# Kernel tuning notes

Measured on AMD Instinct MI355X. Metric: run time of the kernel, lower is better.

## Reference

```python
import jax, jax.numpy as jnp
import numpy as np

B, T, D = 4, 1024, 1024
H = 16                      # attention heads
DS, DC, EXP = 16, 4, 2      # d_state, d_conv, expand
DIN = EXP * D               # 2048
DTR = D // 16               # dt_rank = 64
TOPK_RATIO = 0.25
EPS = 1e-5


def setup_inputs() -> dict:
    key = jax.random.key(0)
    ks = jax.random.split(key, 16)
    def n(k, shape, scale=0.02):
        return jax.random.normal(k, shape, jnp.float32) * scale
    return {
        "x": jax.random.normal(ks[0], (B, T, D), jnp.float32),
        "ln_w": jnp.ones((D,), jnp.float32),
        "ln_b": jnp.zeros((D,), jnp.float32),
        "r_w1": n(ks[1], (D, D // 2)),
        "r_b1": jnp.zeros((D // 2,), jnp.float32),
        "r_w2": n(ks[2], (D // 2, 1)),
        "r_b2": jnp.zeros((1,), jnp.float32),
        "Wq": n(ks[3], (D, D)), "bq": jnp.zeros((D,), jnp.float32),
        "Wk": n(ks[4], (D, D)), "bk": jnp.zeros((D,), jnp.float32),
        "Wv": n(ks[5], (D, D)), "bv": jnp.zeros((D,), jnp.float32),
        "Wo": n(ks[6], (D, D)), "bo": jnp.zeros((D,), jnp.float32),
        "in_w": n(ks[7], (D, 2 * DIN)),
        "conv_w": n(ks[8], (DIN, DC), 0.1),
        "conv_b": jnp.zeros((DIN,), jnp.float32),
        "xproj_w": n(ks[9], (DIN, DTR + 2 * DS)),
        "dt_w": n(ks[10], (DTR, DIN), 0.1),
        "dt_b": jnp.full((DIN,), -4.0, jnp.float32) + n(ks[11], (DIN,), 0.1),
        "A_log": jnp.log(jnp.broadcast_to(jnp.arange(1, DS + 1, dtype=jnp.float32), (DIN, DS))),
        "Dp": jnp.ones((DIN,), jnp.float32),
        "out_w": n(ks[12], (DIN, D)),
    }


def _attn_core(x, Wq, bq, Wk, bk, Wv, bv, Wo, bo):
    b, L, d = x.shape
    hd = d // H
    q = (x @ Wq + bq).reshape(b, L, H, hd)
    k = (x @ Wk + bk).reshape(b, L, H, hd)
    v = (x @ Wv + bv).reshape(b, L, H, hd)
    scores = jnp.einsum('bqhd,bkhd->bhqk', q, k) / jnp.sqrt(jnp.float32(hd))
    p = jax.nn.softmax(scores, axis=-1)
    o = jnp.einsum('bhqk,bkhd->bqhd', p, v).reshape(b, L, d)
    return o @ Wo + bo


def _ssm_core(u, in_w, conv_w, conv_b, xproj_w, dt_w, dt_b, A_log, Dp, out_w):
    # Mamba-style selective SSM on the sub-sequence u: (b, L, D)
    b, L, _ = u.shape
    xi, z = jnp.split(u @ in_w, 2, axis=-1)            # (b, L, DIN) each
    xp = jnp.pad(xi, ((0, 0), (DC - 1, 0), (0, 0)))    # causal depthwise conv1d
    xc = conv_b + sum(xp[:, j:j + L] * conv_w[:, j] for j in range(DC))
    xc = jax.nn.silu(xc)
    proj = xc @ xproj_w                                # (b, L, DTR + 2*DS)
    dtp = proj[..., :DTR]
    Bm = proj[..., DTR:DTR + DS]
    Cm = proj[..., DTR + DS:]
    delta = jax.nn.softplus(dtp @ dt_w + dt_b)         # (b, L, DIN)
    A = -jnp.exp(A_log)                                # (DIN, DS)
    dA = jnp.exp(delta[..., None] * A)                 # (b, L, DIN, DS)
    dBu = (delta * xc)[..., None] * Bm[:, :, None, :]  # (b, L, DIN, DS)

    def step(h, inp):
        dA_t, dBu_t, C_t = inp
        h = dA_t * h + dBu_t                           # (b, DIN, DS)
        return h, jnp.einsum('bds,bs->bd', h, C_t)

    xs = (jnp.moveaxis(dA, 1, 0), jnp.moveaxis(dBu, 1, 0), jnp.moveaxis(Cm, 1, 0))
    _, ys = jax.lax.scan(step, jnp.zeros((b, DIN, DS), u.dtype), xs)
    y = jnp.moveaxis(ys, 0, 1) + xc * Dp               # (b, L, DIN)
    y = y * jax.nn.silu(z)
    return y @ out_w


def reference(x, ln_w, ln_b, r_w1, r_b1, r_w2, r_b2, Wq, bq, Wk, bk, Wv, bv, Wo, bo,
              in_w, conv_w, conv_b, xproj_w, dt_w, dt_b, A_log, Dp, out_w):
    b, t, d = x.shape
    k = min(max(1, int(TOPK_RATIO * t)), t)            # static top-k count
    # pre-norm (LayerNorm)
    mu = x.mean(-1, keepdims=True)
    var = ((x - mu) ** 2).mean(-1, keepdims=True)
    xn = (x - mu) * jax.lax.rsqrt(var + EPS) * ln_w + ln_b
    # router scores (b, t) and top-k dispatch
    scores = jnp.squeeze(jax.nn.gelu(xn @ r_w1 + r_b1) @ r_w2 + r_b2, -1)
    _, topk_idx = jax.lax.top_k(scores, k)
    bidx = jnp.arange(b)[:, None]
    mask = jnp.zeros((b, t), bool).at[bidx, topk_idx].set(True)
    # unselected positions in ascending order (stable sort of 0/1 mask)
    order = jnp.argsort(mask.astype(jnp.int32), axis=1)
    bottom_idx = order[:, :t - k]
    # SSM branch on bottom (t-k) tokens, order-preserving
    x_ssm = xn[bidx, bottom_idx]                       # (b, t-k, d)
    d_ssm_tok = _ssm_core(x_ssm, in_w, conv_w, conv_b, xproj_w, dt_w, dt_b, A_log, Dp, out_w)
    delta_ssm = jnp.zeros_like(xn).at[bidx, bottom_idx].set(d_ssm_tok)
    # attention branch on top-k tokens only (sparse attention)
    x_attn = xn[bidx, topk_idx]                        # (b, k, d)
    d_attn_tok = _attn_core(x_attn, Wq, bq, Wk, bk, Wv, bv, Wo, bo)
    delta_attn = jnp.zeros_like(xn).at[bidx, topk_idx].set(d_attn_tok)
    # masked merge + residual
    delta = jnp.where(mask[..., None], delta_attn, delta_ssm)
    return x + delta
```

## Files before the change

kernel.cpp:

```cpp
#include <hip/hip_runtime.h>
#include <hip/hip_bf16.h>
#include <cstdint>
#include <cstddef>

typedef unsigned short u16;
typedef __attribute__((ext_vector_type(8))) short short8;
typedef __attribute__((ext_vector_type(4))) float f32x4;

__device__ __forceinline__ float b2f(u16 h){ union{unsigned u; float f;} c; c.u = ((unsigned)h)<<16; return c.f; }
__device__ __forceinline__ u16 f2b(float f){ union{float f; unsigned u;} c; c.f = f; unsigned u = c.u; return (u16)((u + 0x7fffu + ((u>>16)&1u)) >> 16); }
__device__ __forceinline__ float gelu_f(float x){
  float x3 = x*x*x;
  return 0.5f*x*(1.f + tanhf(0.7978845608028654f*(x + 0.044715f*x3)));
}
__device__ __forceinline__ void gload_lds16(const void* g, void* l){
  __builtin_amdgcn_global_load_lds((const __attribute__((address_space(1))) void*)g,
                                   (__attribute__((address_space(3))) void*)l, 16, 0, 0);
}

__global__ __launch_bounds__(256) void k_ln(const float* __restrict__ x, const float* __restrict__ w,
    const float* __restrict__ b, float* __restrict__ xn)
{
  int t = blockIdx.x, tid = threadIdx.x;
  float4 v = ((const float4*)(x + (size_t)t*1024))[tid];
  float s = v.x+v.y+v.z+v.w;
  #pragma unroll
  for (int o=32;o;o>>=1) s += __shfl_xor(s,o,64);
  __shared__ float r1[4], r2[4];
  if ((tid&63)==0) r1[tid>>6] = s;
  __syncthreads();
  float mu = (r1[0]+r1[1]+r1[2]+r1[3]) * (1.f/1024.f);
  float4 c = {v.x-mu, v.y-mu, v.z-mu, v.w-mu};
  float q = c.x*c.x+c.y*c.y+c.z*c.z+c.w*c.w;
  #pragma unroll
  for (int o=32;o;o>>=1) q += __shfl_xor(q,o,64);
  if ((tid&63)==0) r2[tid>>6] = q;
  __syncthreads();
  float inv = rsqrtf((r2[0]+r2[1]+r2[2]+r2[3])*(1.f/1024.f) + 1e-5f);
  float4 wv = ((const float4*)w)[tid];
  float4 bv = ((const float4*)b)[tid];
  float4 o4 = {c.x*inv*wv.x+bv.x, c.y*inv*wv.y+bv.y, c.z*inv*wv.z+bv.z, c.w*inv*wv.w+bv.w};
  ((float4*)(xn + (size_t)t*1024))[tid] = o4;
}

__global__ __launch_bounds__(256) void k_tcvt(const float* __restrict__ src, u16* __restrict__ dst, int R, int C)
{
  __shared__ float tile[32][33];
  int c0 = blockIdx.x*32, r0 = blockIdx.y*32;
  int lc = threadIdx.x & 31, lr = threadIdx.x >> 5;
  #pragma unroll
  for (int rr=0; rr<4; rr++) tile[lr + rr*8][lc] = src[(size_t)(r0 + lr + rr*8)*C + c0 + lc];
  __syncthreads();
  #pragma unroll
  for (int rr=0; rr<4; rr++) dst[(size_t)(c0 + lr + rr*8)*R + r0 + lc] = f2b(tile[lc][lr + rr*8]);
}

__global__ __launch_bounds__(256) void k_bpack(const float* __restrict__ bq, const float* __restrict__ bk,
    const float* __restrict__ bv, float* __restrict__ o)
{
  int i = blockIdx.x*256 + threadIdx.x;
  o[i] = (i < 1024) ? bq[i] : ((i < 2048) ? bk[i-1024] : bv[i-2048]);
}

__global__ __launch_bounds__(256) void k_splitA(const float* __restrict__ xn, u16* __restrict__ ap)
{
  int id = blockIdx.x*256 + threadIdx.x;
  int t = id >> 10, k = id & 1023;
  float x = xn[id];
  u16 hi = f2b(x);
  u16 lo = f2b(x - b2f(hi));
  u16* row = ap + (size_t)t*3072;
  row[k] = hi; row[1024+k] = hi; row[2048+k] = lo;
}

__global__ __launch_bounds__(256) void k_splitB(const float* __restrict__ w1, u16* __restrict__ bp)
{
  __shared__ float tile[32][33];
  int n0 = blockIdx.x*32, k0 = blockIdx.y*32;
  int lc = threadIdx.x & 31, lr = threadIdx.x >> 5;
  #pragma unroll
  for (int rr=0; rr<4; rr++) tile[lr+rr*8][lc] = w1[(size_t)(k0+lr+rr*8)*512 + n0+lc];
  __syncthreads();
  #pragma unroll
  for (int rr=0; rr<4; rr++){
    int n = n0 + lr + rr*8, k = k0 + lc;
    float x = tile[lc][lr+rr*8];
    u16 hi = f2b(x);
    u16 lo = f2b(x - b2f(hi));
    u16* row = bp + (size_t)n*3072;
    row[k] = hi; row[1024+k] = lo; row[2048+k] = hi;
  }
}

__global__ __launch_bounds__(256) void k_score(const float* __restrict__ h, const float* __restrict__ w2,
    const float* __restrict__ b2, float* __restrict__ scores)
{
  int tok = blockIdx.x*4 + (threadIdx.x >> 6);
  int lane = threadIdx.x & 63;
  const float* hr = h + (size_t)tok*512;
  float s = 0.f;
  #pragma unroll
  for (int i=0;i<8;i++) s += hr[lane + i*64] * w2[lane + i*64];
  #pragma unroll
  for (int o=32;o;o>>=1) s += __shfl_xor(s, o, 64);
  if (lane==0) scores[tok] = s + b2[0];
}

__global__ __launch_bounds__(1024) void k_topk(const float* __restrict__ scores, int* __restrict__ aidx, int* __restrict__ sidx)
{
  int b = blockIdx.x, tid = threadIdx.x;
  __shared__ float s[1024];
  __shared__ int pf[1024];
  s[tid] = scores[b*1024 + tid];
  __syncthreads();
  float my = s[tid];
  int cnt = 0;
  for (int j=0;j<1024;j++){ float sj = s[j]; cnt += (sj > my) || (sj == my && j < tid); }
  int isa = (cnt < 256) ? 1 : 0;
  pf[tid] = isa; __syncthreads();
  for (int o=1;o<1024;o<<=1){
    int add = (tid >= o) ? pf[tid-o] : 0;
    __syncthreads();
    pf[tid] += add;
    __syncthreads();
  }
  int excl = pf[tid] - isa;
  if (isa) aidx[b*256 + excl] = tid;
  else     sidx[b*768 + (tid - excl)] = tid;
}

__global__ __launch_bounds__(256) void k_gather(const float* __restrict__ xn, const int* __restrict__ aidx,
    const int* __restrict__ sidx, u16* __restrict__ xat, u16* __restrict__ xst)
{
  int id = blockIdx.x;
  int b = id >> 10, s = id & 1023;
  int src; u16* dst;
  if (s < 256) { src = aidx[b*256 + s]; dst = xat + (size_t)(b*256 + s)*1024; }
  else { int ss = s - 256; src = sidx[b*768 + ss]; dst = xst + (size_t)(b*768 + ss)*1024; }
  const float4* sp = (const float4*)(xn + ((size_t)b*1024 + src)*1024);
  int tid = threadIdx.x;
  float4 vv = sp[tid];
  union { u16 u[4]; uint2 d; } pk;
  pk.u[0]=f2b(vv.x); pk.u[1]=f2b(vv.y); pk.u[2]=f2b(vv.z); pk.u[3]=f2b(vv.w);
  ((uint2*)dst)[tid] = pk.d;
}

template<int BM, int BN>
__global__ __launch_bounds__(256) void k_mfma(const u16* __restrict__ A, int lda,
    const u16* __restrict__ Bt, int ldb, const float* __restrict__ bias,
    float* __restrict__ outf, u16* __restrict__ outb, int M, int N, int K,
    int act, int split)
{
  constexpr int WTM = BM/2, WTN = BN/2;
  constexpr int MI = WTM/16, NJ = WTN/16;
  __shared__ u16 lA[2][BM*32];
  __shared__ u16 lB[2][BN*32];
  const int tid = threadIdx.x;
  const int lane = tid & 63;
  const int wv = tid >> 6;
  const int wm = wv >> 1, wn = wv & 1;
  const int tm = blockIdx.x * BM, tn = blockIdx.y * BN;
  const int r0 = lane & 15;
  const int kg = lane >> 4;

  const int ksl = K / gridDim.z;
  const int kbeg = blockIdx.z * ksl;
  if (gridDim.z > 1) outf += (size_t)blockIdx.z * ((size_t)M * N);

  auto stage = [&](int buf, int kt){
    for (int c = tid; c < BM*4; c += 256) {
      int row = c >> 2, j = c & 3;
      int jj = j ^ ((row >> 1) & 3);
      gload_lds16(&A[(size_t)(tm + row)*lda + kt + jj*8], &lA[buf][c*8]);
    }
    for (int c = tid; c < BN*4; c += 256) {
      int row = c >> 2, j = c & 3;
      int jj = j ^ ((row >> 1) & 3);
      gload_lds16(&Bt[(size_t)(tn + row)*ldb + kt + jj*8], &lB[buf][c*8]);
    }
  };

  f32x4 acc[MI][NJ];
  #pragma unroll
  for (int i=0;i<MI;i++)
    #pragma unroll
    for (int j=0;j<NJ;j++) acc[i][j] = (f32x4){0.f,0.f,0.f,0.f};

  stage(0, kbeg);
  __syncthreads();
  const int nk = ksl / 32;
  int cur = 0;
  for (int t = 0; t < nk; t++) {
    if (t + 1 < nk) stage(cur ^ 1, kbeg + (t+1)*32);
    short8 av[MI], bvv[NJ];
    #pragma unroll
    for (int i=0;i<MI;i++){
      int row = wm*WTM + i*16 + r0;
      av[i] = *(const short8*)&lA[cur][row*32 + ((kg ^ ((row>>1)&3))<<3)];
    }
    #pragma unroll
    for (int j=0;j<NJ;j++){
      int row = wn*WTN + j*16 + r0;
      bvv[j] = *(const short8*)&lB[cur][row*32 + ((kg ^ ((row>>1)&3))<<3)];
    }
    #pragma unroll
    for (int i=0;i<MI;i++)
      #pragma unroll
      for (int j=0;j<NJ;j++)
        acc[i][j] = __builtin_amdgcn_mfma_f32_16x16x32_bf16(av[i], bvv[j], acc[i][j], 0, 0, 0);
    __syncthreads();
    cur ^= 1;
  }

  const int rr = kg * 4;
  #pragma unroll
  for (int i=0;i<MI;i++){
    #pragma unroll
    for (int j=0;j<NJ;j++){
      #pragma unroll
      for (int r=0;r<4;r++){
        int row = tm + wm*WTM + i*16 + rr + r;
        int col = tn + wn*WTN + j*16 + r0;
        float v = acc[i][j][r];
        if (bias) v += bias[col];
        if (act == 1) v = (v > 15.f) ? v : log1pf(__expf(v));
        else if (act == 2) v = gelu_f(v);
        if (col < split) outf[(size_t)row*split + col] = v;
        else             outb[(size_t)row*(N-split) + (col-split)] = f2b(v);
      }
    }
  }
}

__global__ __launch_bounds__(256) void k_psum(const float* __restrict__ p, float* __restrict__ o,
    u16* __restrict__ dtpb)
{
  int i = blockIdx.x*256 + threadIdx.x;
  float v = p[i] + p[i+294912] + p[i+589824] + p[i+884736];
  o[i] = v;
  int tok = i / 96, col = i - tok*96;
  if (col < 64) dtpb[tok*64 + col] = f2b(v);
}

__global__ __launch_bounds__(256) void k_attn2(const u16* __restrict__ qkv, u16* __restrict__ ob)
{
  __shared__ u16 lKP[16384];
  __shared__ u16 lVt[16384];
  char* KP = (char*)lKP;
  char* VT = (char*)lVt;
  const int tid = threadIdx.x;
  const int lane = tid & 63;
  const int w = tid >> 6;
  const int bx = blockIdx.x;
  const int b = bx >> 6, h = (bx >> 2) & 15, ch = bx & 3;

  const u16* kbase = qkv + (size_t)(b*256)*3072 + 1024 + h*64;
  const u16* vbase = qkv + (size_t)(b*256)*3072 + 2048 + h*64;

  {
    int rr = tid >> 3;
    int c8 = (tid & 7) * 8;
    for (int i = 0; i < 8; i++) {
      int row = i*32 + rr;
      int4 kv = *(const int4*)&kbase[(size_t)row*3072 + c8];
      int koff = row*128 + c8*2;
      *(int4*)(KP + (koff ^ ((row & 7) << 4))) = kv;
      int4 vv = *(const int4*)&vbase[(size_t)row*3072 + c8];
      union { int4 q; u16 u[8]; } vu; vu.q = vv;
      #pragma unroll
      for (int jj = 0; jj < 8; jj++) {
        int j = (jj + rr) & 7;
        int d = c8 + j;
        int voff = d*512 + row*2;
        *(u16*)(VT + (voff ^ ((d & 7) << 4))) = vu.u[j];
      }
    }
  }

  const int r0 = lane & 15;
  const int kg = lane >> 4;
  const int qrow = ch*64 + w*16 + r0;
  const u16* qp = qkv + (size_t)(b*256 + qrow)*3072 + h*64 + kg*8;
  short8 qf0 = *(const short8*)(qp);
  short8 qf1 = *(const short8*)(qp + 32);

  __syncthreads();

  f32x4 acc[16];
  #pragma unroll
  for (int t = 0; t < 16; t++) acc[t] = (f32x4){0.f,0.f,0.f,0.f};
  #pragma unroll
  for (int t = 0; t < 16; t++) {
    int row = t*16 + r0;
    int base = row*128 + kg*16;
    short8 kf0 = *(const short8*)(KP + ((base     ) ^ ((row & 7) << 4)));
    short8 kf1 = *(const short8*)(KP + ((base + 64) ^ ((row & 7) << 4)));
    acc[t] = __builtin_amdgcn_mfma_f32_16x16x32_bf16(qf0, kf0, acc[t], 0, 0, 0);
    acc[t] = __builtin_amdgcn_mfma_f32_16x16x32_bf16(qf1, kf1, acc[t], 0, 0, 0);
  }

  #pragma unroll
  for (int t = 0; t < 16; t++) acc[t] = acc[t] * 0.125f;
  float lsum[4];
  #pragma unroll
  for (int r = 0; r < 4; r++) {
    float mx = -1e30f;
    #pragma unroll
    for (int t = 0; t < 16; t++) mx = fmaxf(mx, acc[t][r]);
    #pragma unroll
    for (int o = 1; o < 16; o <<= 1) mx = fmaxf(mx, __shfl_xor(mx, o, 64));
    float s = 0.f;
    #pragma unroll
    for (int t = 0; t < 16; t++) { float p = __expf(acc[t][r] - mx); acc[t][r] = p; s += p; }
    #pragma unroll
    for (int o = 1; o < 16; o <<= 1) s += __shfl_xor(s, o, 64);
    lsum[r] = s;
  }

  __syncthreads();
  char* PW = KP + w*8192;
  #pragma unroll
  for (int t = 0; t < 16; t++) {
    int col = t*16 + r0;
    #pragma unroll
    for (int r = 0; r < 4; r++) {
      int row = kg*4 + r;
      int off = row*512 + col*2;
      *(u16*)(PW + (off ^ ((row & 7) << 4))) = f2b(acc[t][r]);
    }
  }

  f32x4 oacc[4];
  #pragma unroll
  for (int dt = 0; dt < 4; dt++) oacc[dt] = (f32x4){0.f,0.f,0.f,0.f};
  #pragma unroll
  for (int kc = 0; kc < 8; kc++) {
    int pbase = r0*512 + kc*64 + kg*16;
    short8 pf = *(const short8*)(PW + (pbase ^ ((r0 & 7) << 4)));
    #pragma unroll
    for (int dt = 0; dt < 4; dt++) {
      int vrow = dt*16 + r0;
      int vb2 = vrow*512 + kc*64 + kg*16;
      short8 vf = *(const short8*)(VT + (vb2 ^ ((vrow & 7) << 4)));
      oacc[dt] = __builtin_amdgcn_mfma_f32_16x16x32_bf16(pf, vf, oacc[dt], 0, 0, 0);
    }
  }

  u16* op = ob + (size_t)(b*256 + ch*64 + w*16)*1024 + h*64;
  #pragma unroll
  for (int dt = 0; dt < 4; dt++) {
    #pragma unroll
    for (int r = 0; r < 4; r++) {
      int row = kg*4 + r;
      float v = oacc[dt][r] / lsum[r];
      op[(size_t)row*1024 + dt*16 + r0] = f2b(v);
    }
  }
}

__global__ __launch_bounds__(256) void k_conv(const float* __restrict__ xi, const float* __restrict__ cw,
    const float* __restrict__ cb, float* __restrict__ xc, u16* __restrict__ xcb)
{
  size_t idx = (size_t)blockIdx.x*256 + threadIdx.x;
  int d = (int)(idx & 2047);
  size_t bt = idx >> 11;
  int t = (int)(bt % 768);
  float acc = cb[d];
  const float* p = xi + idx;
  float w0=cw[d*4+0], w1=cw[d*4+1], w2=cw[d*4+2], w3=cw[d*4+3];
  acc += w3 * p[0];
  if (t >= 1) acc += w2 * p[-2048];
  if (t >= 2) acc += w1 * p[-4096];
  if (t >= 3) acc += w0 * p[-6144];
  float sv = acc / (1.f + __expf(-acc));
  xc[idx]  = sv;
  xcb[idx] = f2b(sv);
}

__global__ __launch_bounds__(256) void k_scan1(const float* __restrict__ delta, const float* __restrict__ xc,
    const float* __restrict__ proj, const float* __restrict__ A_log, float* __restrict__ cs)
{
  int bid = blockIdx.x;
  int db = bid & 7;
  int c  = (bid >> 3) & 15;
  int b  = bid >> 7;
  int d  = db*256 + threadIdx.x;
  float Ar[16];
  #pragma unroll
  for (int s=0;s<16;s++) Ar[s] = -__expf(A_log[d*16+s]);
  float ap[16], hc[16];
  #pragma unroll
  for (int s=0;s<16;s++){ ap[s]=1.f; hc[s]=0.f; }
  size_t row0 = (size_t)b*768 + c*48;
  for (int t=0;t<48;t++){
    size_t row = row0 + t;
    float dl = delta[row*2048 + d];
    float xv = xc[row*2048 + d];
    float du = dl*xv;
    const float4* bp = (const float4*)&proj[row*96 + 64];
    float4 b0 = bp[0], b1 = bp[1], b2 = bp[2], b3 = bp[3];
    float Bc[16] = {b0.x,b0.y,b0.z,b0.w,b1.x,b1.y,b1.z,b1.w,
                    b2.x,b2.y,b2.z,b2.w,b3.x,b3.y,b3.z,b3.w};
    #pragma unroll
    for (int s=0;s<16;s++){
      float dA = __expf(dl*Ar[s]);
      ap[s] *= dA;
      hc[s] = dA*hc[s] + du*Bc[s];
    }
  }
  size_t base = ((size_t)(b*16 + c)*32)*2048 + d;
  #pragma unroll
  for (int s=0;s<16;s++){
    cs[base + (size_t)s*2048]      = ap[s];
    cs[base + (size_t)(16+s)*2048] = hc[s];
  }
}

__global__ __launch_bounds__(256) void k_scan2(float* __restrict__ cs)
{
  int bid = blockIdx.x;
  int db = bid & 7;
  int s  = (bid >> 3) & 15;
  int b  = bid >> 7;
  int d  = db*256 + threadIdx.x;
  float h = 0.f;
  for (int c=0;c<16;c++){
    size_t base = ((size_t)(b*16 + c)*32)*2048 + d;
    float ap = cs[base + (size_t)s*2048];
    float hc = cs[base + (size_t)(16+s)*2048];
    cs[base + (size_t)(16+s)*2048] = h;
    h = ap*h + hc;
  }
}

__global__ __launch_bounds__(256) void k_scan3(const float* __restrict__ delta, const float* __restrict__ xc,
    const float* __restrict__ proj, const float* __restrict__ cs, const u16* __restrict__ zb,
    const float* __restrict__ A_log, const float* __restrict__ Dp, u16* __restrict__ yb)
{
  int bid = blockIdx.x;
  int db = bid & 7;
  int c  = (bid >> 3) & 15;
  int b  = bid >> 7;
  int d  = db*256 + threadIdx.x;
  float Ar[16];
  #pragma unroll
  for (int s=0;s<16;s++) Ar[s] = -__expf(A_log[d*16+s]);
  float dpv = Dp[d];
  float h[16];
  size_t base = ((size_t)(b*16 + c)*32)*2048 + d;
  #pragma unroll
  for (int s=0;s<16;s++) h[s] = cs[base + (size_t)(16+s)*2048];
  size_t row0 = (size_t)b*768 + c*48;
  for (int t=0;t<48;t++){
    size_t row = row0 + t;
    float dl = delta[row*2048 + d];
    float xv = xc[row*2048 + d];
    float du = dl*xv;
    const float4* bp = (const float4*)&proj[row*96 + 64];
    float4 b0 = bp[0], b1 = bp[1], b2 = bp[2], b3 = bp[3];
    const float4* cp = (const float4*)&proj[row*96 + 80];
    float4 c0 = cp[0], c1 = cp[1], c2 = cp[2], c3 = cp[3];
    float Bc[16] = {b0.x,b0.y,b0.z,b0.w,b1.x,b1.y,b1.z,b1.w,
                    b2.x,b2.y,b2.z,b2.w,b3.x,b3.y,b3.z,b3.w};
    float Cc[16] = {c0.x,c0.y,c0.z,c0.w,c1.x,c1.y,c1.z,c1.w,
                    c2.x,c2.y,c2.z,c2.w,c3.x,c3.y,c3.z,c3.w};
    float y = 0.f;
    #pragma unroll
    for (int s=0;s<16;s++){
      float dA = __expf(dl*Ar[s]);
      h[s] = dA*h[s] + du*Bc[s];
      y += h[s]*Cc[s];
    }
    y += xv*dpv;
    float z = b2f(zb[row*2048 + d]);
    float g = z / (1.f + __expf(-z));
    yb[row*2048 + d] = f2b(y*g);
  }
}

__global__ __launch_bounds__(256) void k_scat(const float* __restrict__ x, const int* __restrict__ idxarr,
    const float* __restrict__ dlt, float* __restrict__ out, int per_b)
{
  int id = blockIdx.x;
  int b = id / per_b;
  int t = idxarr[id];
  const float4* xp = (const float4*)(x + ((size_t)b*1024 + t)*1024);
  const float4* dp = (const float4*)(dlt + (size_t)id*1024);
  float4* op = (float4*)(out + ((size_t)b*1024 + t)*1024);
  int tid = threadIdx.x;
  float4 a = xp[tid], d = dp[tid];
  op[tid] = (float4){a.x+d.x, a.y+d.y, a.z+d.z, a.w+d.w};
}

extern "C" void kernel_launch(void* const* d_in, const int* in_sizes, int n_in,
                              void* d_out, int out_size, void* d_ws, size_t ws_size,
                              hipStream_t stream)
{
  const float* x      = (const float*)d_in[0];
  const float* ln_w   = (const float*)d_in[1];
  const float* ln_b   = (const float*)d_in[2];
  const float* r_w1   = (const float*)d_in[3];
  const float* r_b1   = (const float*)d_in[4];
  const float* r_w2   = (const float*)d_in[5];
  const float* r_b2   = (const float*)d_in[6];
  const float* Wq     = (const float*)d_in[7];
  const float* bq     = (const float*)d_in[8];
  const float* Wk     = (const float*)d_in[9];
  const float* bk     = (const float*)d_in[10];
  const float* Wv     = (const float*)d_in[11];
  const float* bv     = (const float*)d_in[12];
  const float* Wo     = (const float*)d_in[13];
  const float* bo     = (const float*)d_in[14];
  const float* in_w   = (const float*)d_in[15];
  const float* conv_w = (const float*)d_in[16];
  const float* conv_b = (const float*)d_in[17];
  const float* xproj_w= (const float*)d_in[18];
  const float* dt_w   = (const float*)d_in[19];
  const float* dt_b   = (const float*)d_in[20];
  const float* A_log  = (const float*)d_in[21];
  const float* Dp     = (const float*)d_in[22];
  const float* out_w  = (const float*)d_in[23];
  float* out = (float*)d_out;

  uint8_t* ws = (uint8_t*)d_ws;
  size_t off = 0;
  auto alloc = [&](size_t bytes)->uint8_t*{
    uint8_t* p = ws + off;
    off += (bytes + 255) & ~(size_t)255;
    return p;
  };

  float* xn    = (float*)alloc(4096ull*1024*4);
  u16*   wqt   = (u16*)  alloc(1024ull*1024*2);
  u16*   wkt   = (u16*)  alloc(1024ull*1024*2);
  u16*   wvt   = (u16*)  alloc(1024ull*1024*2);
  u16*   wot   = (u16*)  alloc(1024ull*1024*2);
  u16*   inwt  = (u16*)  alloc(4096ull*1024*2);
  u16*   outwt = (u16*)  alloc(1024ull*2048*2);
  u16*   xpwt  = (u16*)  alloc(96ull*2048*2);
  u16*   dtwt  = (u16*)  alloc(2048ull*64*2);
  u16*   r1pk  = (u16*)  alloc(512ull*3072*2);
  float* scores= (float*)alloc(4096*4);
  int*   aidx  = (int*)  alloc(1024*4);
  int*   sidx  = (int*)  alloc(3072*4);
  u16*   xat   = (u16*)  alloc(1024ull*1024*2);
  u16*   xst   = (u16*)  alloc(3072ull*1024*2);
  float* qkvb  = (float*)alloc(3072*4);

  float* s_projp = xn;
  float* cs = xn;

  uint8_t* arena = ws + off;
  float* h  = (float*)arena;
  u16*   apk = (u16*)(arena + 8388608);
  u16*   qkvbuf = (u16*)(arena);
  u16*   obuf   = (u16*)(arena + 6291456);
  float* adelta = (float*)(arena + 8388608);
  float* s_xi   = (float*)(arena);
  u16*   s_zb   = (u16*)(arena + 25165824);
  float* s_xc   = (float*)(arena + 37748736);
  u16*   s_xcb  = (u16*)(arena + 62914560);
  float* s_proj = (float*)(arena + 75497472);
  u16*   s_dtpb = (u16*)(arena + 76677120);
  float* s_delta  = s_xi;
  u16*   s_yb     = s_xcb;
  float* s_sdelta = (float*)s_zb;

  hipLaunchKernelGGL(k_ln, dim3(4096), dim3(256), 0, stream, x, ln_w, ln_b, xn);
  hipLaunchKernelGGL(k_tcvt, dim3(32,32),  dim3(256), 0, stream, Wq,     wqt,   1024, 1024);
  hipLaunchKernelGGL(k_tcvt, dim3(32,32),  dim3(256), 0, stream, Wk,     wkt,   1024, 1024);
  hipLaunchKernelGGL(k_tcvt, dim3(32,32),  dim3(256), 0, stream, Wv,     wvt,   1024, 1024);
  hipLaunchKernelGGL(k_tcvt, dim3(32,32),  dim3(256), 0, stream, Wo,     wot,   1024, 1024);
  hipLaunchKernelGGL(k_tcvt, dim3(128,32), dim3(256), 0, stream, in_w,   inwt,  1024, 4096);
  hipLaunchKernelGGL(k_tcvt, dim3(32,64),  dim3(256), 0, stream, out_w,  outwt, 2048, 1024);
  hipLaunchKernelGGL(k_tcvt, dim3(3,64),   dim3(256), 0, stream, xproj_w,xpwt,  2048, 96);
  hipLaunchKernelGGL(k_tcvt, dim3(64,2),   dim3(256), 0, stream, dt_w,   dtwt,  64,   2048);
  hipLaunchKernelGGL(k_bpack, dim3(12), dim3(256), 0, stream, bq, bk, bv, qkvb);
  hipLaunchKernelGGL(k_splitB, dim3(16,32), dim3(256), 0, stream, r_w1, r1pk);
  hipLaunchKernelGGL(k_splitA, dim3(16384), dim3(256), 0, stream, xn, apk);
  hipLaunchKernelGGL((k_mfma<64,128>), dim3(64,4), dim3(256), 0, stream,
      apk, 3072, r1pk, 3072, r_b1, h, (u16*)nullptr, 4096, 512, 3072, 2, 512);
  hipLaunchKernelGGL(k_score, dim3(1024), dim3(256), 0, stream, h, r_w2, r_b2, scores);
  hipLaunchKernelGGL(k_topk, dim3(4), dim3(1024), 0, stream, scores, aidx, sidx);
  hipLaunchKernelGGL(k_gather, dim3(4096), dim3(256), 0, stream, xn, aidx, sidx, xat, xst);
  hipLaunchKernelGGL((k_mfma<64,128>), dim3(16,24), dim3(256), 0, stream,
      xat, 1024, wqt, 1024, qkvb, (float*)nullptr, qkvbuf, 1024, 3072, 1024, 0, 0);
  hipLaunchKernelGGL(k_attn2, dim3(256), dim3(256), 0, stream, qkvbuf, obuf);
  hipLaunchKernelGGL((k_mfma<64,64>), dim3(16,16), dim3(256), 0, stream,
      obuf, 1024, wot, 1024, bo, adelta, (u16*)nullptr, 1024, 1024, 1024, 0, 1024);
  hipLaunchKernelGGL(k_scat, dim3(1024), dim3(256), 0, stream, x, aidx, adelta, out, 256);
  hipLaunchKernelGGL((k_mfma<128,128>), dim3(24,32), dim3(256), 0, stream,
      xst, 1024, inwt, 1024, (const float*)nullptr, s_xi, s_zb, 3072, 4096, 1024, 0, 2048);
  hipLaunchKernelGGL(k_conv, dim3(24576), dim3(256), 0, stream, s_xi, conv_w, conv_b, s_xc, s_xcb);
  hipLaunchKernelGGL((k_mfma<64,96>), dim3(48,1,4), dim3(256), 0, stream,
      s_xcb, 2048, xpwt, 2048, (const float*)nullptr, s_projp, (u16*)nullptr, 3072, 96, 2048, 0, 96);
  hipLaunchKernelGGL(k_psum, dim3(1152), dim3(256), 0, stream, s_projp, s_proj, s_dtpb);
  hipLaunchKernelGGL((k_mfma<128,128>), dim3(24,16), dim3(256), 0, stream,
      s_dtpb, 64, dtwt, 64, dt_b, s_delta, (u16*)nullptr, 3072, 2048, 64, 1, 2048);
  hipLaunchKernelGGL(k_scan1, dim3(512), dim3(256), 0, stream, s_delta, s_xc, s_proj, A_log, cs);
  hipLaunchKernelGGL(k_scan2, dim3(512), dim3(256), 0, stream, cs);
  hipLaunchKernelGGL(k_scan3, dim3(512), dim3(256), 0, stream, s_delta, s_xc, s_proj, cs, s_zb, A_log, Dp, s_yb);
  hipLaunchKernelGGL((k_mfma<64,128>), dim3(48,8), dim3(256), 0, stream,
      s_yb, 2048, outwt, 2048, (const float*)nullptr, s_sdelta, (u16*)nullptr, 3072, 1024, 2048, 0, 1024);
  hipLaunchKernelGGL(k_scat, dim3(3072), dim3(256), 0, stream, x, sidx, s_sdelta, out, 768);
}
```

Before: 492.4 us.

## Fuse router GELU and score dot into GEMM epilogue, retile GEMMs, vectorize splitA

The router GEMM epilogue now applies GELU, multiplies by r_w2 and reduces across columns, writing per-column-block partial scores. A small kernel sums the partials, which removes the 4096x512 hidden activation write and read. Several GEMMs move to smaller M tiles to launch more blocks, and splitA processes four elements per thread with vector stores. The extra partial-sum pass and the smaller tiles give up some per-block data reuse in exchange for more parallelism.

```diff
diff --git a/kernel.cpp b/kernel.cpp
--- a/kernel.cpp
+++ b/kernel.cpp
@@ -64,13 +64,17 @@
 
 __global__ __launch_bounds__(256) void k_splitA(const float* __restrict__ xn, u16* __restrict__ ap)
 {
-  int id = blockIdx.x*256 + threadIdx.x;
-  int t = id >> 10, k = id & 1023;
-  float x = xn[id];
-  u16 hi = f2b(x);
-  u16 lo = f2b(x - b2f(hi));
+  int t = blockIdx.x;
+  int k4 = threadIdx.x*4;
+  float4 v = *(const float4*)&xn[(size_t)t*1024 + k4];
+  union{u16 u[4]; uint2 d;} hi, lo;
+  float xs[4] = {v.x, v.y, v.z, v.w};
+  #pragma unroll
+  for (int e=0;e<4;e++){ u16 h = f2b(xs[e]); hi.u[e]=h; lo.u[e]=f2b(xs[e]-b2f(h)); }
   u16* row = ap + (size_t)t*3072;
-  row[k] = hi; row[1024+k] = hi; row[2048+k] = lo;
+  *(uint2*)&row[k4]      = hi.d;
+  *(uint2*)&row[1024+k4] = hi.d;
+  *(uint2*)&row[2048+k4] = lo.d;
 }
 
 __global__ __launch_bounds__(256) void k_splitB(const float* __restrict__ w1, u16* __restrict__ bp)
@@ -92,18 +96,14 @@
   }
 }
 
-__global__ __launch_bounds__(256) void k_score(const float* __restrict__ h, const float* __restrict__ w2,
-    const float* __restrict__ b2, float* __restrict__ scores)
-{
-  int tok = blockIdx.x*4 + (threadIdx.x >> 6);
-  int lane = threadIdx.x & 63;
-  const float* hr = h + (size_t)tok*512;
-  float s = 0.f;
-  #pragma unroll
-  for (int i=0;i<8;i++) s += hr[lane + i*64] * w2[lane + i*64];
-  #pragma unroll
-  for (int o=32;o;o>>=1) s += __shfl_xor(s, o, 64);
-  if (lane==0) scores[tok] = s + b2[0];
+__global__ __launch_bounds__(256) void k_score3(const float* __restrict__ ps, const float* __restrict__ b2,
+    float* __restrict__ scores)
+{
+  int i = blockIdx.x*256 + threadIdx.x;
+  float s = b2[0];
+  #pragma unroll
+  for (int p=0;p<16;p++) s += ps[p*4096 + i];
+  scores[i] = s;
 }
 
 __global__ __launch_bounds__(1024) void k_topk(const float* __restrict__ scores, int* __restrict__ aidx, int* __restrict__ sidx)
@@ -210,6 +210,27 @@
         acc[i][j] = __builtin_amdgcn_mfma_f32_16x16x32_bf16(av[i], bvv[j], acc[i][j], 0, 0, 0);
     __syncthreads();
     cur ^= 1;
+  }
+
+  if (act == 3) {
+    const float* w2 = (const float*)outb;
+    #pragma unroll
+    for (int i=0;i<MI;i++){
+      #pragma unroll
+      for (int r=0;r<4;r++){
+        float t = 0.f;
+        #pragma unroll
+        for (int j=0;j<NJ;j++){
+          int col = tn + wn*WTN + j*16 + r0;
+          t += gelu_f(acc[i][j][r] + bias[col]) * w2[col];
+        }
+        #pragma unroll
+        for (int o=1;o<16;o<<=1) t += __shfl_xor(t, o, 64);
+        if (r0 == 0)
+          outf[(size_t)(blockIdx.y*2 + wn)*M + tm + wm*WTM + i*16 + kg*4 + r] = t;
+      }
+    }
+    return;
   }
 
   const int rr = kg * 4;
@@ -551,8 +572,8 @@
   float* cs = xn;
 
   uint8_t* arena = ws + off;
-  float* h  = (float*)arena;
-  u16*   apk = (u16*)(arena + 8388608);
+  u16*   apk = (u16*)(arena);
+  float* ps  = (float*)(arena + 25165824);
   u16*   qkvbuf = (u16*)(arena);
   u16*   obuf   = (u16*)(arena + 6291456);
   float* adelta = (float*)(arena + 8388608);
@@ -577,30 +598,30 @@
   hipLaunchKernelGGL(k_tcvt, dim3(64,2),   dim3(256), 0, stream, dt_w,   dtwt,  64,   2048);
   hipLaunchKernelGGL(k_bpack, dim3(12), dim3(256), 0, stream, bq, bk, bv, qkvb);
   hipLaunchKernelGGL(k_splitB, dim3(16,32), dim3(256), 0, stream, r_w1, r1pk);
-  hipLaunchKernelGGL(k_splitA, dim3(16384), dim3(256), 0, stream, xn, apk);
-  hipLaunchKernelGGL((k_mfma<64,128>), dim3(64,4), dim3(256), 0, stream,
-      apk, 3072, r1pk, 3072, r_b1, h, (u16*)nullptr, 4096, 512, 3072, 2, 512);
-  hipLaunchKernelGGL(k_score, dim3(1024), dim3(256), 0, stream, h, r_w2, r_b2, scores);
+  hipLaunchKernelGGL(k_splitA, dim3(4096), dim3(256), 0, stream, xn, apk);
+  hipLaunchKernelGGL((k_mfma<64,64>), dim3(64,8), dim3(256), 0, stream,
+      apk, 3072, r1pk, 3072, r_b1, ps, (u16*)r_w2, 4096, 512, 3072, 3, 0);
+  hipLaunchKernelGGL(k_score3, dim3(16), dim3(256), 0, stream, ps, r_b2, scores);
   hipLaunchKernelGGL(k_topk, dim3(4), dim3(1024), 0, stream, scores, aidx, sidx);
   hipLaunchKernelGGL(k_gather, dim3(4096), dim3(256), 0, stream, xn, aidx, sidx, xat, xst);
-  hipLaunchKernelGGL((k_mfma<64,128>), dim3(16,24), dim3(256), 0, stream,
+  hipLaunchKernelGGL((k_mfma<32,128>), dim3(32,24), dim3(256), 0, stream,
       xat, 1024, wqt, 1024, qkvb, (float*)nullptr, qkvbuf, 1024, 3072, 1024, 0, 0);
   hipLaunchKernelGGL(k_attn2, dim3(256), dim3(256), 0, stream, qkvbuf, obuf);
-  hipLaunchKernelGGL((k_mfma<64,64>), dim3(16,16), dim3(256), 0, stream,
+  hipLaunchKernelGGL((k_mfma<32,64>), dim3(32,16), dim3(256), 0, stream,
       obuf, 1024, wot, 1024, bo, adelta, (u16*)nullptr, 1024, 1024, 1024, 0, 1024);
   hipLaunchKernelGGL(k_scat, dim3(1024), dim3(256), 0, stream, x, aidx, adelta, out, 256);
   hipLaunchKernelGGL((k_mfma<128,128>), dim3(24,32), dim3(256), 0, stream,
       xst, 1024, inwt, 1024, (const float*)nullptr, s_xi, s_zb, 3072, 4096, 1024, 0, 2048);
   hipLaunchKernelGGL(k_conv, dim3(24576), dim3(256), 0, stream, s_xi, conv_w, conv_b, s_xc, s_xcb);
-  hipLaunchKernelGGL((k_mfma<64,96>), dim3(48,1,4), dim3(256), 0, stream,
+  hipLaunchKernelGGL((k_mfma<32,96>), dim3(96,1,4), dim3(256), 0, stream,
       s_xcb, 2048, xpwt, 2048, (const float*)nullptr, s_projp, (u16*)nullptr, 3072, 96, 2048, 0, 96);
   hipLaunchKernelGGL(k_psum, dim3(1152), dim3(256), 0, stream, s_projp, s_proj, s_dtpb);
-  hipLaunchKernelGGL((k_mfma<128,128>), dim3(24,16), dim3(256), 0, stream,
+  hipLaunchKernelGGL((k_mfma<64,128>), dim3(48,16), dim3(256), 0, stream,
       s_dtpb, 64, dtwt, 64, dt_b, s_delta, (u16*)nullptr, 3072, 2048, 64, 1, 2048);
   hipLaunchKernelGGL(k_scan1, dim3(512), dim3(256), 0, stream, s_delta, s_xc, s_proj, A_log, cs);
   hipLaunchKernelGGL(k_scan2, dim3(512), dim3(256), 0, stream, cs);
   hipLaunchKernelGGL(k_scan3, dim3(512), dim3(256), 0, stream, s_delta, s_xc, s_proj, cs, s_zb, A_log, Dp, s_yb);
-  hipLaunchKernelGGL((k_mfma<64,128>), dim3(48,8), dim3(256), 0, stream,
+  hipLaunchKernelGGL((k_mfma<32,128>), dim3(96,8), dim3(256), 0, stream,
       s_yb, 2048, outwt, 2048, (const float*)nullptr, s_sdelta, (u16*)nullptr, 3072, 1024, 2048, 0, 1024);
   hipLaunchKernelGGL(k_scat, dim3(3072), dim3(256), 0, stream, x, sidx, s_sdelta, out, 768);
 }
```

Result: faster. 436.0 us (-11.5%).
